# Kernel tuning notes

Hardware: AMD Instinct MI355X
Metric: run time of the kernel (lower is better)

## Reference

```python
import jax, jax.numpy as jnp
import numpy as np

NUM_EXPERTS = 64
TOP_K = 8
NORM_TOPK_PROB = True


def setup_inputs() -> dict:
    key = jax.random.key(0)
    k1, k2 = jax.random.split(key)
    hidden_states = jax.random.normal(k1, (8192, 4096), dtype=jnp.float32)
    gate_w = jax.random.normal(k2, (NUM_EXPERTS, 4096), dtype=jnp.float32) * (1.0 / np.sqrt(4096))
    return {"hidden_states": hidden_states, "gate_w": gate_w}


def reference(hidden_states, gate_w):
    # router_logits: (T, E) = hidden @ gate_w.T
    router_logits = jnp.einsum('th,eh->te', hidden_states, gate_w)
    # softmax in float32 (matches F.softmax(..., dtype=torch.float32))
    router_probs = jax.nn.softmax(router_logits.astype(jnp.float32), axis=-1)
    # top-k selection (descending, like torch.topk)
    expert_weights, expert_indices = jax.lax.top_k(router_probs, TOP_K)
    if NORM_TOPK_PROB:
        expert_weights = expert_weights / jnp.sum(expert_weights, axis=-1, keepdims=True)
    expert_weights = expert_weights.astype(hidden_states.dtype)
    # load-balancing loss: N_e * sum_i f_i * p_i
    num_tokens = router_probs.shape[0]
    one_hot = jax.nn.one_hot(expert_indices, NUM_EXPERTS, dtype=jnp.float32)  # (T, K, E)
    tokens_per_expert = one_hot.sum(axis=(0, 1))                              # (E,)
    f = tokens_per_expert / (num_tokens * TOP_K)
    p = router_probs.mean(axis=0)
    aux_loss = NUM_EXPERTS * jnp.sum(f * p)
    return (expert_weights, expert_indices, aux_loss)
```

## Files before the change

### kernel.cpp

```cpp
#include <hip/hip_runtime.h>
#include <math.h>

#define HDIM 4096
#define NEXP 64
#define NTOK 8192
#define KSPLIT 8
#define KSLICE (HDIM / KSPLIT)
#define NCHUNK (KSLICE / 32)
#define NKC (HDIM / 32)
#define AUXF 1024
#define TPW 2
#define BT_TERM (NKC * 4 * 64 * 8)
#define BT_KC (4 * 64 * 8)

typedef short short8 __attribute__((ext_vector_type(8)));
typedef float f32x4 __attribute__((ext_vector_type(4)));

union i4s8 { int4 i; short8 s; };

__device__ __forceinline__ void split2x3(float x0, float x1, int& h, int& md, int& lo) {
  unsigned u0 = __float_as_uint(x0), u1 = __float_as_uint(x1);
  unsigned h0 = u0 & 0xFFFF0000u, h1 = u1 & 0xFFFF0000u;
  float r0 = x0 - __uint_as_float(h0);
  float r1 = x1 - __uint_as_float(h1);
  unsigned m0 = __float_as_uint(r0) & 0xFFFF0000u;
  unsigned m1 = __float_as_uint(r1) & 0xFFFF0000u;
  float s0 = r0 - __uint_as_float(m0);
  float s1 = r1 - __uint_as_float(m1);
  h  = (int)((h0 >> 16) | h1);
  md = (int)((m0 >> 16) | m1);
  lo = (int)((__float_as_uint(s0) >> 16) | (__float_as_uint(s1) & 0xFFFF0000u));
}

__device__ __forceinline__ void split8(const float4& p0, const float4& p1,
                                       short8& h8, short8& m8, short8& l8) {
  i4s8 h, m, l;
  split2x3(p0.x, p0.y, h.i.x, m.i.x, l.i.x);
  split2x3(p0.z, p0.w, h.i.y, m.i.y, l.i.y);
  split2x3(p1.x, p1.y, h.i.z, m.i.z, l.i.z);
  split2x3(p1.z, p1.w, h.i.w, m.i.w, l.i.w);
  h8 = h.s; m8 = m.s; l8 = l.s;
}

__global__ __launch_bounds__(256) void prep_k(const float* __restrict__ W,
                                              short* __restrict__ Bs,
                                              float* __restrict__ auxbuf) {
  if (blockIdx.x == 128) {
#pragma unroll
    for (int j = 0; j < 4; ++j) auxbuf[j * 256 + threadIdx.x] = 0.f;
    return;
  }
  const int g = blockIdx.x * 256 + threadIdx.x;
  const int n = g >> 9;
  const int k8 = g & 511;
  const float4 p0 = *(const float4*)&W[(size_t)n * HDIM + k8 * 8];
  const float4 p1 = *(const float4*)&W[(size_t)n * HDIM + k8 * 8 + 4];
  short8 h8, m8, l8;
  split8(p0, p1, h8, m8, l8);
  const int kc = k8 >> 2, quad = k8 & 3;
  const size_t o = (((size_t)kc * 4 + quad) * 64 + n) * 8;
  *(short8*)&Bs[o] = h8;
  *(short8*)&Bs[o + BT_TERM] = m8;
  *(short8*)&Bs[o + 2 * BT_TERM] = l8;
}

__global__ __launch_bounds__(256, 4) void gemm_k(const float* __restrict__ A,
                                                 const short* __restrict__ Bs,
                                                 float* __restrict__ Lp,
                                                 int atomic_mode) {
  const int tid = threadIdx.x;
  const int wave = tid >> 6, lane = tid & 63;
  const int l15 = lane & 15, quad = lane >> 4;
  const int m_base = blockIdx.x * 64 + wave * 16;
  const int kb = blockIdx.y;
  float* Lout = Lp + (atomic_mode ? (size_t)0 : (size_t)kb * NTOK * NEXP);

  const float* a0 = A + (size_t)(m_base + l15) * HDIM + kb * KSLICE + quad * 8;
  const short* bbase = Bs + ((size_t)(kb * NCHUNK) * 4 + quad) * 512 + l15 * 8;

  f32x4 acc[4];
#pragma unroll
  for (int nt = 0; nt < 4; ++nt) acc[nt] = (f32x4){0.f, 0.f, 0.f, 0.f};

  float4 ra[2][2];
  auto loadA = [&](int buf, int i) {
    ra[buf][0] = *(const float4*)(a0 + i * 32);
    ra[buf][1] = *(const float4*)(a0 + i * 32 + 4);
  };

  short8 fa_cur[3], fa_next[3];
  loadA(0, 0);
  loadA(1, 1);
  split8(ra[0][0], ra[0][1], fa_cur[0], fa_cur[1], fa_cur[2]);

#pragma unroll 2
  for (int i = 0; i < NCHUNK; ++i) {
    const short* bc = bbase + (size_t)i * BT_KC;
    short8 bh[4], bm[4], bl[4];
#pragma unroll
    for (int nt = 0; nt < 4; ++nt) {
      bh[nt] = *(const short8*)(bc + nt * 128);
      bm[nt] = *(const short8*)(bc + nt * 128 + BT_TERM);
      bl[nt] = *(const short8*)(bc + nt * 128 + 2 * BT_TERM);
    }
    if (i + 2 < NCHUNK) loadA(i & 1, i + 2);
    if (i + 1 < NCHUNK)
      split8(ra[(i + 1) & 1][0], ra[(i + 1) & 1][1],
             fa_next[0], fa_next[1], fa_next[2]);
#pragma unroll
    for (int nt = 0; nt < 4; ++nt) {
      f32x4 c = acc[nt];
      c = __builtin_amdgcn_mfma_f32_16x16x32_bf16(fa_cur[0], bh[nt], c, 0, 0, 0);
      c = __builtin_amdgcn_mfma_f32_16x16x32_bf16(fa_cur[0], bm[nt], c, 0, 0, 0);
      c = __builtin_amdgcn_mfma_f32_16x16x32_bf16(fa_cur[1], bh[nt], c, 0, 0, 0);
      c = __builtin_amdgcn_mfma_f32_16x16x32_bf16(fa_cur[0], bl[nt], c, 0, 0, 0);
      c = __builtin_amdgcn_mfma_f32_16x16x32_bf16(fa_cur[2], bh[nt], c, 0, 0, 0);
      c = __builtin_amdgcn_mfma_f32_16x16x32_bf16(fa_cur[1], bm[nt], c, 0, 0, 0);
      acc[nt] = c;
    }
#pragma unroll
    for (int r = 0; r < 3; ++r) fa_cur[r] = fa_next[r];
  }

#pragma unroll
  for (int nt = 0; nt < 4; ++nt)
#pragma unroll
    for (int r = 0; r < 4; ++r) {
      const int m = m_base + quad * 4 + r;
      const int n = nt * 16 + l15;
      if (atomic_mode) atomicAdd(&Lout[(size_t)m * NEXP + n], acc[nt][r]);
      else Lout[(size_t)m * NEXP + n] = acc[nt][r];
    }
}

__global__ __launch_bounds__(256) void topk_k(const float* __restrict__ Lp, int nsl,
                                              float* __restrict__ out,
                                              float* __restrict__ auxbuf) {
  __shared__ float sl[4][64];
  __shared__ float s_aux[128];
  const int tid = threadIdx.x;
  const int wave = tid >> 6, lane = tid & 63;
  if (tid < 128) s_aux[tid] = 0.f;
  __syncthreads();

  for (int it = 0; it < TPW; ++it) {
    const int t = (blockIdx.x * 4 + wave) * TPW + it;
    float x = 0.f;
    for (int s = 0; s < nsl; ++s)
      x += Lp[(size_t)s * (NTOK * NEXP) + (size_t)t * NEXP + lane];
    sl[wave][lane] = x;

    float mx = x;
#pragma unroll
    for (int off = 32; off >= 1; off >>= 1)
      mx = fmaxf(mx, __shfl_xor(mx, off, 64));
    const float e = __expf(x - mx);
    float ssum = e;
#pragma unroll
    for (int off = 32; off >= 1; off >>= 1) ssum += __shfl_xor(ssum, off, 64);
    const float prob = e / ssum;

    __syncthreads();

    int cnt = 0;
#pragma unroll
    for (int c = 0; c < 4; ++c) {
      const float4 v0 = *(const float4*)&sl[wave][c * 16 + 0];
      const float4 v1 = *(const float4*)&sl[wave][c * 16 + 4];
      const float4 v2 = *(const float4*)&sl[wave][c * 16 + 8];
      const float4 v3 = *(const float4*)&sl[wave][c * 16 + 12];
      const float xv[16] = {v0.x, v0.y, v0.z, v0.w, v1.x, v1.y, v1.z, v1.w,
                            v2.x, v2.y, v2.z, v2.w, v3.x, v3.y, v3.z, v3.w};
#pragma unroll
      for (int j = 0; j < 16; ++j) {
        const int jj = c * 16 + j;
        cnt += (xv[j] > x) || (xv[j] == x && jj < lane);
      }
    }

    float tp = (cnt < 8) ? prob : 0.f;
    float tsum = tp;
#pragma unroll
    for (int off = 32; off >= 1; off >>= 1) tsum += __shfl_xor(tsum, off, 64);

    const int dst = cnt << 2;
    const float pv = __uint_as_float(
        (unsigned)__builtin_amdgcn_ds_permute(dst, (int)__float_as_uint(prob)));
    const int pi = __builtin_amdgcn_ds_permute(dst, lane);
    if (lane < 8) {
      out[(size_t)t * 8 + lane] = pv / tsum;
      out[(size_t)NTOK * 8 + (size_t)t * 8 + lane] = (float)pi;
    }
    atomicAdd(&s_aux[lane], prob);
    if (cnt < 8) atomicAdd(&s_aux[64 + lane], 1.f);
  }
  __syncthreads();
  if (tid < 128) atomicAdd(&auxbuf[(blockIdx.x & 7) * 128 + tid], s_aux[tid]);
}

__global__ void aux_k(const float* __restrict__ auxbuf, float* __restrict__ out) {
  const int e = threadIdx.x;
  float p = 0.f, f = 0.f;
#pragma unroll
  for (int c = 0; c < 8; ++c) {
    p += auxbuf[c * 128 + e];
    f += auxbuf[c * 128 + 64 + e];
  }
  p *= (1.f / (float)NTOK);
  f *= (1.f / ((float)NTOK * 8.f));
  float v = f * p;
#pragma unroll
  for (int off = 32; off >= 1; off >>= 1) v += __shfl_xor(v, off, 64);
  if (e == 0) out[2 * NTOK * 8] = 64.f * v;
}

extern "C" void kernel_launch(void* const* d_in, const int* in_sizes, int n_in,
                              void* d_out, int out_size, void* d_ws, size_t ws_size,
                              hipStream_t stream) {
  const float* hidden = (const float*)d_in[0];
  const float* gate = (const float*)d_in[1];
  float* out = (float*)d_out;
  float* ws = (float*)d_ws;
  float* auxbuf = ws;

  const size_t full_need =
      (size_t)AUXF * 4 + (size_t)KSPLIT * NTOK * NEXP * 4 + (size_t)3 * BT_TERM * 2;
  const int atomic_mode = (ws_size < full_need) ? 1 : 0;
  const int nsl = atomic_mode ? 1 : KSPLIT;
  float* slices = ws + AUXF;
  short* Bs = (short*)(ws + AUXF + (size_t)nsl * NTOK * NEXP);

  if (atomic_mode)
    hipMemsetAsync(slices, 0, (size_t)NTOK * NEXP * 4, stream);

  prep_k<<<129, 256, 0, stream>>>(gate, Bs, auxbuf);
  gemm_k<<<dim3(128, KSPLIT), 256, 0, stream>>>(hidden, Bs, slices, atomic_mode);
  topk_k<<<NTOK / (4 * TPW), 256, 0, stream>>>(slices, nsl, out, auxbuf);
  aux_k<<<1, 64, 0, stream>>>(auxbuf, out);
}
```

Measured before the change: 238.1 us.

## Halve K-split, double-buffer B fragments, and use nontemporal A loads

The GEMM's K-split drops from 8 to 4, so there are half as many blocks and each one runs twice as many K chunks. The B fragments for the next chunk are now prefetched into a double-buffered register array while the current chunk runs its MFMAs, and the A loads use nontemporal hints. Launch bounds fall from 4 to 3 waves per SIMD to leave room for the extra registers. This aims to hide B-load latency and cut partial-slice traffic and the reduction in topk, at the cost of lower occupancy and fewer blocks (512) to spread across the CUs.

New measurement: 240.5 us. No clear change (+1.0%).

```diff
diff --git a/kernel.cpp b/kernel.cpp
--- a/kernel.cpp
+++ b/kernel.cpp
@@ -4,7 +4,7 @@
 #define HDIM 4096
 #define NEXP 64
 #define NTOK 8192
-#define KSPLIT 8
+#define KSPLIT 4
 #define KSLICE (HDIM / KSPLIT)
 #define NCHUNK (KSLICE / 32)
 #define NKC (HDIM / 32)
@@ -32,8 +32,8 @@
   lo = (int)((__float_as_uint(s0) >> 16) | (__float_as_uint(s1) & 0xFFFF0000u));
 }
 
-__device__ __forceinline__ void split8(const float4& p0, const float4& p1,
-                                       short8& h8, short8& m8, short8& l8) {
+__device__ __forceinline__ void split8v(const f32x4& p0, const f32x4& p1,
+                                        short8& h8, short8& m8, short8& l8) {
   i4s8 h, m, l;
   split2x3(p0.x, p0.y, h.i.x, m.i.x, l.i.x);
   split2x3(p0.z, p0.w, h.i.y, m.i.y, l.i.y);
@@ -53,10 +53,10 @@
   const int g = blockIdx.x * 256 + threadIdx.x;
   const int n = g >> 9;
   const int k8 = g & 511;
-  const float4 p0 = *(const float4*)&W[(size_t)n * HDIM + k8 * 8];
-  const float4 p1 = *(const float4*)&W[(size_t)n * HDIM + k8 * 8 + 4];
+  const f32x4 p0 = *(const f32x4*)&W[(size_t)n * HDIM + k8 * 8];
+  const f32x4 p1 = *(const f32x4*)&W[(size_t)n * HDIM + k8 * 8 + 4];
   short8 h8, m8, l8;
-  split8(p0, p1, h8, m8, l8);
+  split8v(p0, p1, h8, m8, l8);
   const int kc = k8 >> 2, quad = k8 & 3;
   const size_t o = (((size_t)kc * 4 + quad) * 64 + n) * 8;
   *(short8*)&Bs[o] = h8;
@@ -64,7 +64,20 @@
   *(short8*)&Bs[o + 2 * BT_TERM] = l8;
 }
 
-__global__ __launch_bounds__(256, 4) void gemm_k(const float* __restrict__ A,
+__device__ __forceinline__ f32x4 ntload4(const float* p) {
+  return __builtin_nontemporal_load((const f32x4*)p);
+}
+
+__device__ __forceinline__ void loadB(const short* bc, short8* b) {
+#pragma unroll
+  for (int nt = 0; nt < 4; ++nt) {
+    b[nt]     = *(const short8*)(bc + nt * 128);
+    b[4 + nt] = *(const short8*)(bc + nt * 128 + BT_TERM);
+    b[8 + nt] = *(const short8*)(bc + nt * 128 + 2 * BT_TERM);
+  }
+}
+
+__global__ __launch_bounds__(256, 3) void gemm_k(const float* __restrict__ A,
                                                  const short* __restrict__ Bs,
                                                  float* __restrict__ Lp,
                                                  int atomic_mode) {
@@ -82,44 +95,37 @@
 #pragma unroll
   for (int nt = 0; nt < 4; ++nt) acc[nt] = (f32x4){0.f, 0.f, 0.f, 0.f};
 
-  float4 ra[2][2];
-  auto loadA = [&](int buf, int i) {
-    ra[buf][0] = *(const float4*)(a0 + i * 32);
-    ra[buf][1] = *(const float4*)(a0 + i * 32 + 4);
-  };
-
-  short8 fa_cur[3], fa_next[3];
-  loadA(0, 0);
-  loadA(1, 1);
-  split8(ra[0][0], ra[0][1], fa_cur[0], fa_cur[1], fa_cur[2]);
+  short8 B[2][12];
+  f32x4 ra[2][2];
+  short8 fa[3];
+
+  loadB(bbase, B[0]);
+  ra[0][0] = ntload4(a0);
+  ra[0][1] = ntload4(a0 + 4);
+  ra[1][0] = ntload4(a0 + 32);
+  ra[1][1] = ntload4(a0 + 36);
 
 #pragma unroll 2
   for (int i = 0; i < NCHUNK; ++i) {
-    const short* bc = bbase + (size_t)i * BT_KC;
-    short8 bh[4], bm[4], bl[4];
-#pragma unroll
-    for (int nt = 0; nt < 4; ++nt) {
-      bh[nt] = *(const short8*)(bc + nt * 128);
-      bm[nt] = *(const short8*)(bc + nt * 128 + BT_TERM);
-      bl[nt] = *(const short8*)(bc + nt * 128 + 2 * BT_TERM);
-    }
-    if (i + 2 < NCHUNK) loadA(i & 1, i + 2);
-    if (i + 1 < NCHUNK)
-      split8(ra[(i + 1) & 1][0], ra[(i + 1) & 1][1],
-             fa_next[0], fa_next[1], fa_next[2]);
+    const int cur = i & 1;
+    const int ip1 = (i + 1 < NCHUNK) ? i + 1 : i;
+    loadB(bbase + (size_t)ip1 * BT_KC, B[cur ^ 1]);
+    split8v(ra[cur][0], ra[cur][1], fa[0], fa[1], fa[2]);
+    if (i + 2 < NCHUNK) {
+      ra[cur][0] = ntload4(a0 + (i + 2) * 32);
+      ra[cur][1] = ntload4(a0 + (i + 2) * 32 + 4);
+    }
 #pragma unroll
     for (int nt = 0; nt < 4; ++nt) {
       f32x4 c = acc[nt];
-      c = __builtin_amdgcn_mfma_f32_16x16x32_bf16(fa_cur[0], bh[nt], c, 0, 0, 0);
-      c = __builtin_amdgcn_mfma_f32_16x16x32_bf16(fa_cur[0], bm[nt], c, 0, 0, 0);
-      c = __builtin_amdgcn_mfma_f32_16x16x32_bf16(fa_cur[1], bh[nt], c, 0, 0, 0);
-      c = __builtin_amdgcn_mfma_f32_16x16x32_bf16(fa_cur[0], bl[nt], c, 0, 0, 0);
-      c = __builtin_amdgcn_mfma_f32_16x16x32_bf16(fa_cur[2], bh[nt], c, 0, 0, 0);
-      c = __builtin_amdgcn_mfma_f32_16x16x32_bf16(fa_cur[1], bm[nt], c, 0, 0, 0);
+      c = __builtin_amdgcn_mfma_f32_16x16x32_bf16(fa[0], B[cur][nt], c, 0, 0, 0);
+      c = __builtin_amdgcn_mfma_f32_16x16x32_bf16(fa[0], B[cur][4 + nt], c, 0, 0, 0);
+      c = __builtin_amdgcn_mfma_f32_16x16x32_bf16(fa[1], B[cur][nt], c, 0, 0, 0);
+      c = __builtin_amdgcn_mfma_f32_16x16x32_bf16(fa[0], B[cur][8 + nt], c, 0, 0, 0);
+      c = __builtin_amdgcn_mfma_f32_16x16x32_bf16(fa[2], B[cur][nt], c, 0, 0, 0);
+      c = __builtin_amdgcn_mfma_f32_16x16x32_bf16(fa[1], B[cur][4 + nt], c, 0, 0, 0);
       acc[nt] = c;
     }
-#pragma unroll
-    for (int r = 0; r < 3; ++r) fa_cur[r] = fa_next[r];
   }
 
 #pragma unroll
@@ -224,14 +230,14 @@
   float* auxbuf = ws;
 
   const size_t full_need =
-      (size_t)AUXF * 4 + (size_t)KSPLIT * NTOK * NEXP * 4 + (size_t)3 * BT_TERM * 2;
+      (size_t)AUXF * 4 + (size_t)KSPLIT * NTOK * NEXP * 4 + (size_t)3 * BT_TERM * 2 + 4096;
   const int atomic_mode = (ws_size < full_need) ? 1 : 0;
   const int nsl = atomic_mode ? 1 : KSPLIT;
   float* slices = ws + AUXF;
   short* Bs = (short*)(ws + AUXF + (size_t)nsl * NTOK * NEXP);
 
   if (atomic_mode)
-    hipMemsetAsync(slices, 0, (size_t)NTOK * NEXP * 4, stream);
+    (void)hipMemsetAsync(slices, 0, (size_t)NTOK * NEXP * 4, stream);
 
   prep_k<<<129, 256, 0, stream>>>(gate, Bs, auxbuf);
   gemm_k<<<dim3(128, KSPLIT), 256, 0, stream>>>(hidden, Bs, slices, atomic_mode);
```
